# Kernel optimization log

Measured on AMD Instinct MI355X. Metric: run time of the kernel, lower is better.

Reference implementation:

```python
import jax, jax.numpy as jnp
import numpy as np
from jax import lax

B, C, H, W = 16, 256, 56, 56
MID = 16  # SE: max(C//16, 4)
EPS = 1e-5


def _bn(x, g, b, m, v):
    # inference-mode BatchNorm2d folded to per-channel scale/shift
    s = g * lax.rsqrt(v + EPS)
    return x * s[None, :, None, None] + (b - m * s)[None, :, None, None]


def _dw(x, w, ph, pw):
    # depthwise conv, NCHW, kernel w: [C,1,kh,kw]
    return lax.conv_general_dilated(
        x, w, window_strides=(1, 1), padding=[(ph, ph), (pw, pw)],
        dimension_numbers=('NCHW', 'OIHW', 'NCHW'), feature_group_count=C)


def _pw(x, w):
    # 1x1 conv, w: [O,C,1,1]
    return jnp.einsum('bchw,oc->bohw', x, w[:, :, 0, 0])


def _se(x, w1, b1, w2, b2):
    s = x.mean(axis=(2, 3))                      # [B,C] squeeze
    s = jax.nn.relu(s @ w1.T + b1)               # [B,MID]
    s = jax.nn.sigmoid(s @ w2.T + b2)            # [B,C]
    return x * s[:, :, None, None]


def setup_inputs() -> dict:
    key = jax.random.key(0)
    ks = jax.random.split(key, 32)
    rn = lambda i, shape, sc=0.05: jax.random.normal(ks[i], shape, jnp.float32) * sc
    ru = lambda i, shape: jax.random.uniform(ks[i], shape, jnp.float32)
    return {
        'x': rn(0, (B, C, H, W), 1.0),
        'pw1_w': rn(1, (C, C, 1, 1)),
        'xy3_w': rn(2, (C, 1, 3, 3)), 'xy5_w': rn(3, (C, 1, 5, 5)),
        'bnxy_g': ru(4, (C,)), 'bnxy_b': rn(5, (C,)), 'bnxy_m': rn(6, (C,)), 'bnxy_v': ru(7, (C,)),
        'xz3_w': rn(8, (C, 1, 1, 3)), 'xz5_w': rn(9, (C, 1, 1, 5)),
        'bnxz_g': ru(10, (C,)), 'bnxz_b': rn(11, (C,)), 'bnxz_m': rn(12, (C,)), 'bnxz_v': ru(13, (C,)),
        'yz3_w': rn(14, (C, 1, 3, 1)), 'yz5_w': rn(15, (C, 1, 5, 1)),
        'bnyz_g': ru(16, (C,)), 'bnyz_b': rn(17, (C,)), 'bnyz_m': rn(18, (C,)), 'bnyz_v': ru(19, (C,)),
        'alpha': jnp.full((1, C, 1, 1), 0.5, jnp.float32),
        'beta': jnp.full((1, C, 1, 1), 0.5, jnp.float32),
        'pw2_w': rn(20, (C, C, 1, 1)),
        'bn2_g': ru(21, (C,)), 'bn2_b': rn(22, (C,)), 'bn2_m': rn(23, (C,)), 'bn2_v': ru(24, (C,)),
        'fc1_w': rn(25, (MID, C)), 'fc1_b': rn(26, (MID,)),
        'fc2_w': rn(27, (C, MID)), 'fc2_b': rn(28, (C,)),
    }


def reference(x, pw1_w, xy3_w, xy5_w, bnxy_g, bnxy_b, bnxy_m, bnxy_v,
              xz3_w, xz5_w, bnxz_g, bnxz_b, bnxz_m, bnxz_v,
              yz3_w, yz5_w, bnyz_g, bnyz_b, bnyz_m, bnyz_v,
              alpha, beta, pw2_w, bn2_g, bn2_b, bn2_m, bn2_v,
              fc1_w, fc1_b, fc2_w, fc2_b):
    # Pw1: 1x1 conv, no BN / no act
    out = _pw(x, pw1_w)
    # MS_TOP (stride=1 -> pool is identity)
    # [B] xy branch: DW 3x3 + DW 5x5 -> BN -> ReLU
    f_xy = jax.nn.relu(_bn(_dw(out, xy3_w, 1, 1) + _dw(out, xy5_w, 2, 2),
                           bnxy_g, bnxy_b, bnxy_m, bnxy_v))
    # [A] xz branch: per-row depthwise Conv1d along W == depthwise (1,k) 2D conv
    f_xz = jax.nn.relu(_bn(_dw(out, xz3_w, 0, 1) + _dw(out, xz5_w, 0, 2),
                           bnxz_g, bnxz_b, bnxz_m, bnxz_v))
    # [A] yz branch: per-column depthwise Conv1d along H == depthwise (k,1) 2D conv
    f_yz = jax.nn.relu(_bn(_dw(out, yz3_w, 1, 0) + _dw(out, yz5_w, 2, 0),
                           bnyz_g, bnyz_b, bnyz_m, bnyz_v))
    # [C] learnable-gate fusion
    gate = jax.nn.sigmoid(alpha * f_xz + beta * f_yz)
    top = jax.nn.relu(f_xy * gate)
    # Pw2: 1x1 conv -> BN -> ReLU
    out2 = jax.nn.relu(_bn(_pw(top, pw2_w), bn2_g, bn2_b, bn2_m, bn2_v))
    # SE channel attention
    out2 = _se(out2, fc1_w, fc1_b, fc2_w, fc2_b)
    # DropPath is identity at inference; shortcut is identity (stride=1, in==out)
    return out2 + x
```

## Files before the change

kernel.cpp:

```cpp
#include <hip/hip_runtime.h>
#include <math.h>

typedef __bf16 bf16;
typedef __bf16 bf16x8 __attribute__((ext_vector_type(8)));
typedef __bf16 bf16x4 __attribute__((ext_vector_type(4)));
typedef float f32x4 __attribute__((ext_vector_type(4)));

#define CC 256
#define BB 16
#define HH 56
#define WW 56
#define HWSZ 3136
#define EPS 1e-5f

#define OFF_SCALE 0
#define OFF_SUMS  16384
#define OFF_WBF1  32768
#define OFF_WBF2  163840
#define OFF_WDW   294912
#define OFF_BNC   312832
#define OFF_OUT2  321024

__global__ __launch_bounds__(256) void precast(
    const float* __restrict__ w1, const float* __restrict__ w2,
    const float* __restrict__ xy3, const float* __restrict__ xy5,
    const float* __restrict__ xz3, const float* __restrict__ xz5,
    const float* __restrict__ yz3, const float* __restrict__ yz5,
    const float* __restrict__ gxy, const float* __restrict__ bxy,
    const float* __restrict__ mxy, const float* __restrict__ vxy,
    const float* __restrict__ gxz, const float* __restrict__ bxz,
    const float* __restrict__ mxz, const float* __restrict__ vxz,
    const float* __restrict__ gyz, const float* __restrict__ byz,
    const float* __restrict__ myz, const float* __restrict__ vyz,
    const float* __restrict__ alpha, const float* __restrict__ beta,
    bf16* __restrict__ wbf1, bf16* __restrict__ wbf2,
    bf16* __restrict__ wdw, float* __restrict__ bnc,
    float* __restrict__ sums)
{
    const int blk = blockIdx.x, t = threadIdx.x;
    if (blk < 128) {
        int i = blk * 512 + t * 2;
        wbf1[i] = (bf16)w1[i]; wbf1[i + 1] = (bf16)w1[i + 1];
    } else if (blk < 256) {
        int i = (blk - 128) * 512 + t * 2;
        wbf2[i] = (bf16)w2[i]; wbf2[i + 1] = (bf16)w2[i + 1];
    } else {
        const int c = t;
#pragma unroll
        for (int dh = 0; dh < 5; ++dh)
#pragma unroll
            for (int dw = 0; dw < 5; ++dw) {
                float v = xy5[c * 25 + dh * 5 + dw];
                if (dh >= 1 && dh <= 3 && dw >= 1 && dw <= 3)
                    v += xy3[c * 9 + (dh - 1) * 3 + (dw - 1)];
                wdw[(dh * 5 + dw) * CC + c] = (bf16)v;
            }
#pragma unroll
        for (int d = 0; d < 5; ++d) {
            float v = xz5[c * 5 + d];
            if (d >= 1 && d <= 3) v += xz3[c * 3 + d - 1];
            wdw[(25 + d) * CC + c] = (bf16)v;
            float u = yz5[c * 5 + d];
            if (d >= 1 && d <= 3) u += yz3[c * 3 + d - 1];
            wdw[(30 + d) * CC + c] = (bf16)u;
        }
        float s;
        s = gxy[c] * rsqrtf(vxy[c] + EPS); bnc[0*CC+c] = s; bnc[1*CC+c] = bxy[c] - mxy[c]*s;
        s = gxz[c] * rsqrtf(vxz[c] + EPS); bnc[2*CC+c] = s; bnc[3*CC+c] = bxz[c] - mxz[c]*s;
        s = gyz[c] * rsqrtf(vyz[c] + EPS); bnc[4*CC+c] = s; bnc[5*CC+c] = byz[c] - myz[c]*s;
        bnc[6*CC+c] = alpha[c]; bnc[7*CC+c] = beta[c];
        for (int i = t; i < BB * CC; i += 256) sums[i] = 0.f;
    }
}

__global__ __launch_bounds__(256, 2) void pw_gemm1(
    const float* __restrict__ in, const bf16* __restrict__ wbf,
    bf16* __restrict__ mid)
{
    __shared__ __align__(16) bf16 XT[64][264];
    const int hw0 = blockIdx.x * 64;
    const int b   = blockIdx.y;
    const int t   = threadIdx.x;
    const int lane = t & 63, wv = t >> 6;
    const int q = lane >> 4, n = lane & 15;
    const int co_w = wv * 64;

    bf16x8 aq[4][8];
#pragma unroll
    for (int cf = 0; cf < 4; ++cf) {
        const bf16* wp = wbf + (size_t)(co_w + cf * 16 + n) * CC + q * 8;
#pragma unroll
        for (int kk = 0; kk < 8; ++kk)
            aq[cf][kk] = *(const bf16x8*)(wp + kk * 32);
    }

    {
        const int hwg = (t & 15) * 4;
        const int cig = (t >> 4) * 4;
        const float* base = in + (size_t)b * CC * HWSZ + hw0 + hwg;
#pragma unroll
        for (int pass = 0; pass < 4; ++pass) {
            const int ci0 = pass * 64 + cig;
            f32x4 v[4];
#pragma unroll
            for (int i = 0; i < 4; ++i)
                v[i] = *(const f32x4*)(base + (size_t)(ci0 + i) * HWSZ);
#pragma unroll
            for (int j = 0; j < 4; ++j) {
                bf16x4 r = {(bf16)v[0][j], (bf16)v[1][j], (bf16)v[2][j], (bf16)v[3][j]};
                *(bf16x4*)(&XT[hwg + j][ci0]) = r;
            }
        }
    }
    __syncthreads();

    f32x4 acc[4][4] = {};
#pragma unroll
    for (int kk = 0; kk < 8; ++kk) {
        bf16x8 bq[4];
#pragma unroll
        for (int hf = 0; hf < 4; ++hf)
            bq[hf] = *(const bf16x8*)(&XT[hf * 16 + n][kk * 32 + q * 8]);
#pragma unroll
        for (int cf = 0; cf < 4; ++cf)
#pragma unroll
            for (int hf = 0; hf < 4; ++hf)
                acc[cf][hf] = __builtin_amdgcn_mfma_f32_16x16x32_bf16(
                    aq[cf][kk], bq[hf], acc[cf][hf], 0, 0, 0);
    }

    bf16* ob = mid + ((size_t)b * HWSZ + hw0) * CC;
#pragma unroll
    for (int cf = 0; cf < 4; ++cf) {
        const int co4 = co_w + cf * 16 + q * 4;
#pragma unroll
        for (int hf = 0; hf < 4; ++hf) {
            bf16x4 r = {(bf16)acc[cf][hf][0], (bf16)acc[cf][hf][1],
                        (bf16)acc[cf][hf][2], (bf16)acc[cf][hf][3]};
            *(bf16x4*)(ob + (size_t)(hf * 16 + n) * CC + co4) = r;
        }
    }
}

__global__ __launch_bounds__(256) void dwfuse(
    const bf16* __restrict__ mid, const bf16* __restrict__ wdw,
    const float* __restrict__ bnc, bf16* __restrict__ top)
{
    __shared__ __align__(16) bf16 lw2[35 * 512];
    const int t = threadIdx.x;
    for (int idx = t; idx < 35 * 64; idx += 256) {
        const int tap = idx >> 6, slot = idx & 63;
        *(bf16x8*)(&lw2[tap * 512 + slot * 8]) =
            *(const bf16x8*)(wdw + tap * 256 + (slot & 31) * 8);
    }
    __syncthreads();

    const int w  = blockIdx.x * 8 + (t >> 5);
    const int h0 = blockIdx.y * 2;
    const int bb = blockIdx.z;
    const int c0 = (t & 31) * 8;
    const int ls = (t & 63) * 8;
    const size_t plane = (size_t)bb * HWSZ;

    float axy[2][8] = {}, axz[2][8] = {}, ayz[2][8] = {};
#pragma unroll
    for (int dhh = 0; dhh < 6; ++dhh) {
        const int hh = h0 - 2 + dhh;
        if ((unsigned)hh >= (unsigned)HH) continue;
#pragma unroll
        for (int dw = 0; dw < 5; ++dw) {
            const int ww = w + dw - 2;
            if ((unsigned)ww >= (unsigned)WW) continue;
            bf16x8 v = *(const bf16x8*)(mid + ((plane + hh * WW + ww) * CC + c0));
            float fv[8];
#pragma unroll
            for (int j = 0; j < 8; ++j) fv[j] = (float)v[j];
#pragma unroll
            for (int p = 0; p < 2; ++p) {
                const int dh = dhh - p;
                if (dh < 0 || dh > 4) continue;
                bf16x8 wc = *(const bf16x8*)(&lw2[(dh * 5 + dw) * 512 + ls]);
#pragma unroll
                for (int j = 0; j < 8; ++j) axy[p][j] += (float)wc[j] * fv[j];
                if (dh == 2) {
                    bf16x8 wz = *(const bf16x8*)(&lw2[(25 + dw) * 512 + ls]);
#pragma unroll
                    for (int j = 0; j < 8; ++j) axz[p][j] += (float)wz[j] * fv[j];
                }
                if (dw == 2) {
                    bf16x8 wy = *(const bf16x8*)(&lw2[(30 + dh) * 512 + ls]);
#pragma unroll
                    for (int j = 0; j < 8; ++j) ayz[p][j] += (float)wy[j] * fv[j];
                }
            }
        }
    }

    float bnv[8][8];
#pragma unroll
    for (int k = 0; k < 8; ++k) {
        f32x4 a0 = *(const f32x4*)(bnc + k * CC + c0);
        f32x4 a1 = *(const f32x4*)(bnc + k * CC + c0 + 4);
#pragma unroll
        for (int j = 0; j < 4; ++j) { bnv[k][j] = a0[j]; bnv[k][4 + j] = a1[j]; }
    }

#pragma unroll
    for (int p = 0; p < 2; ++p) {
        bf16x8 r;
#pragma unroll
        for (int j = 0; j < 8; ++j) {
            const float fxy = fmaxf(axy[p][j] * bnv[0][j] + bnv[1][j], 0.f);
            const float fxz = fmaxf(axz[p][j] * bnv[2][j] + bnv[3][j], 0.f);
            const float fyz = fmaxf(ayz[p][j] * bnv[4][j] + bnv[5][j], 0.f);
            const float z   = bnv[6][j] * fxz + bnv[7][j] * fyz;
            const float g   = 1.f / (1.f + expf(-z));
            r[j] = (bf16)fmaxf(fxy * g, 0.f);
        }
        *(bf16x8*)(top + ((plane + (h0 + p) * WW + w) * CC + c0)) = r;
    }
}

__global__ __launch_bounds__(256, 2) void pw_gemm2(
    const bf16* __restrict__ top, const bf16* __restrict__ wbf,
    const float* __restrict__ g2, const float* __restrict__ b2,
    const float* __restrict__ m2, const float* __restrict__ v2,
    bf16* __restrict__ out2, float* __restrict__ sums)
{
    __shared__ __align__(16) bf16 XT[64][264];
    const int hw0 = blockIdx.x * 64;
    const int b   = blockIdx.y;
    const int t   = threadIdx.x;
    const int lane = t & 63, wv = t >> 6;
    const int q = lane >> 4, n = lane & 15;
    const int co_w = wv * 64;

    bf16x8 aq[4][8];
#pragma unroll
    for (int cf = 0; cf < 4; ++cf) {
        const bf16* wp = wbf + (size_t)(co_w + cf * 16 + n) * CC + q * 8;
#pragma unroll
        for (int kk = 0; kk < 8; ++kk)
            aq[cf][kk] = *(const bf16x8*)(wp + kk * 32);
    }

    {
        const int hw_r = t >> 2;
        const int k0   = (t & 3) * 64;
        const bf16* src = top + ((size_t)b * HWSZ + hw0 + hw_r) * CC + k0;
#pragma unroll
        for (int j = 0; j < 8; ++j)
            *(bf16x8*)(&XT[hw_r][k0 + j * 8]) = *(const bf16x8*)(src + j * 8);
    }
    __syncthreads();

    f32x4 acc[4][4] = {};
#pragma unroll
    for (int kk = 0; kk < 8; ++kk) {
        bf16x8 bq[4];
#pragma unroll
        for (int hf = 0; hf < 4; ++hf)
            bq[hf] = *(const bf16x8*)(&XT[hf * 16 + n][kk * 32 + q * 8]);
#pragma unroll
        for (int cf = 0; cf < 4; ++cf)
#pragma unroll
            for (int hf = 0; hf < 4; ++hf)
                acc[cf][hf] = __builtin_amdgcn_mfma_f32_16x16x32_bf16(
                    aq[cf][kk], bq[hf], acc[cf][hf], 0, 0, 0);
    }

    bf16* ob = out2 + ((size_t)b * HWSZ + hw0) * CC;
#pragma unroll
    for (int cf = 0; cf < 4; ++cf) {
        const int co4 = co_w + cf * 16 + q * 4;
        f32x4 g = *(const f32x4*)(g2 + co4);
        f32x4 bb = *(const f32x4*)(b2 + co4);
        f32x4 mm = *(const f32x4*)(m2 + co4);
        f32x4 vv = *(const f32x4*)(v2 + co4);
        f32x4 sc, sh;
#pragma unroll
        for (int r = 0; r < 4; ++r) {
            sc[r] = g[r] * rsqrtf(vv[r] + EPS);
            sh[r] = bb[r] - mm[r] * sc[r];
        }
        f32x4 rs = {};
#pragma unroll
        for (int hf = 0; hf < 4; ++hf) {
            bf16x4 r4;
#pragma unroll
            for (int r = 0; r < 4; ++r) {
                float v = fmaxf(acc[cf][hf][r] * sc[r] + sh[r], 0.f);
                rs[r] += v;
                r4[r] = (bf16)v;
            }
            *(bf16x4*)(ob + (size_t)(hf * 16 + n) * CC + co4) = r4;
        }
#pragma unroll
        for (int msk = 1; msk < 16; msk <<= 1)
#pragma unroll
            for (int r = 0; r < 4; ++r) rs[r] += __shfl_xor(rs[r], msk);
        if (n == 0) {
#pragma unroll
            for (int r = 0; r < 4; ++r)
                atomicAdd(&sums[b * CC + co4 + r], rs[r]);
        }
    }
}

__global__ __launch_bounds__(256) void se_fc(
    const float* __restrict__ sums,
    const float* __restrict__ w1, const float* __restrict__ b1,
    const float* __restrict__ w2, const float* __restrict__ b2,
    float* __restrict__ scale)
{
    __shared__ float mean[256];
    __shared__ float hid[16];
    const int b = blockIdx.x, tid = threadIdx.x;
    mean[tid] = sums[b * CC + tid] * (1.f / (float)HWSZ);
    __syncthreads();
    if (tid < 16) {
        float h = b1[tid];
        for (int cd = 0; cd < 256; ++cd) h += w1[tid * 256 + cd] * mean[cd];
        hid[tid] = fmaxf(h, 0.f);
    }
    __syncthreads();
    float v = b2[tid];
#pragma unroll
    for (int md = 0; md < 16; ++md) v += w2[tid * 16 + md] * hid[md];
    scale[b * CC + tid] = 1.f / (1.f + expf(-v));
}

__global__ __launch_bounds__(256) void se_apply(
    const bf16* __restrict__ out2, const float* __restrict__ x,
    const float* __restrict__ scale, float* __restrict__ out)
{
    __shared__ float TT[64 * 68];
    const int hw0 = blockIdx.x * 64;
    const int c0  = blockIdx.y * 64;
    const int b   = blockIdx.z;
    const int t   = threadIdx.x;

    {
        const int hw_r = t >> 2;
        const int coff = (t & 3) * 16;
        const bf16* p = out2 + ((size_t)b * HWSZ + hw0 + hw_r) * CC + c0 + coff;
        bf16x8 u0 = *(const bf16x8*)(p);
        bf16x8 u1 = *(const bf16x8*)(p + 8);
        const float* sp = scale + b * CC + c0 + coff;
        f32x4 s0 = *(const f32x4*)(sp), s1 = *(const f32x4*)(sp + 4);
        f32x4 s2 = *(const f32x4*)(sp + 8), s3 = *(const f32x4*)(sp + 12);
#pragma unroll
        for (int j = 0; j < 4; ++j) {
            TT[(coff + j)      * 68 + hw_r] = (float)u0[j]     * s0[j];
            TT[(coff + 4 + j)  * 68 + hw_r] = (float)u0[4 + j] * s1[j];
            TT[(coff + 8 + j)  * 68 + hw_r] = (float)u1[j]     * s2[j];
            TT[(coff + 12 + j) * 68 + hw_r] = (float)u1[4 + j] * s3[j];
        }
    }
    __syncthreads();
    {
        const int c_r   = t >> 2;
        const int hwoff = (t & 3) * 16;
        const size_t go = ((size_t)b * CC + c0 + c_r) * HWSZ + hw0 + hwoff;
#pragma unroll
        for (int v = 0; v < 4; ++v) {
            f32x4 tv = *(const f32x4*)(&TT[c_r * 68 + hwoff + v * 4]);
            f32x4 xv = *(const f32x4*)(x + go + v * 4);
#pragma unroll
            for (int j = 0; j < 4; ++j) tv[j] += xv[j];
            *(f32x4*)(out + go + v * 4) = tv;
        }
    }
}

extern "C" void kernel_launch(void* const* d_in, const int* in_sizes, int n_in,
                              void* d_out, int out_size, void* d_ws, size_t ws_size,
                              hipStream_t stream)
{
    const float* x      = (const float*)d_in[0];
    const float* pw1_w  = (const float*)d_in[1];
    const float* xy3_w  = (const float*)d_in[2];
    const float* xy5_w  = (const float*)d_in[3];
    const float* bnxy_g = (const float*)d_in[4];
    const float* bnxy_b = (const float*)d_in[5];
    const float* bnxy_m = (const float*)d_in[6];
    const float* bnxy_v = (const float*)d_in[7];
    const float* xz3_w  = (const float*)d_in[8];
    const float* xz5_w  = (const float*)d_in[9];
    const float* bnxz_g = (const float*)d_in[10];
    const float* bnxz_b = (const float*)d_in[11];
    const float* bnxz_m = (const float*)d_in[12];
    const float* bnxz_v = (const float*)d_in[13];
    const float* yz3_w  = (const float*)d_in[14];
    const float* yz5_w  = (const float*)d_in[15];
    const float* bnyz_g = (const float*)d_in[16];
    const float* bnyz_b = (const float*)d_in[17];
    const float* bnyz_m = (const float*)d_in[18];
    const float* bnyz_v = (const float*)d_in[19];
    const float* alpha  = (const float*)d_in[20];
    const float* beta   = (const float*)d_in[21];
    const float* pw2_w  = (const float*)d_in[22];
    const float* bn2_g  = (const float*)d_in[23];
    const float* bn2_b  = (const float*)d_in[24];
    const float* bn2_m  = (const float*)d_in[25];
    const float* bn2_v  = (const float*)d_in[26];
    const float* fc1_w  = (const float*)d_in[27];
    const float* fc1_b  = (const float*)d_in[28];
    const float* fc2_w  = (const float*)d_in[29];
    const float* fc2_b  = (const float*)d_in[30];

    const size_t NEL = (size_t)BB * CC * HWSZ;
    char* ws = (char*)d_ws;
    float* scale = (float*)(ws + OFF_SCALE);
    float* sums  = (float*)(ws + OFF_SUMS);
    bf16*  wbf1  = (bf16*) (ws + OFF_WBF1);
    bf16*  wbf2  = (bf16*) (ws + OFF_WBF2);
    bf16*  wdw   = (bf16*) (ws + OFF_WDW);
    float* bnc   = (float*)(ws + OFF_BNC);
    bf16*  out2  = (bf16*) (ws + OFF_OUT2);
    bf16*  mid   = (bf16*)d_out;
    bf16*  top   = (bf16*)d_out + NEL;

    precast<<<257, 256, 0, stream>>>(pw1_w, pw2_w,
        xy3_w, xy5_w, xz3_w, xz5_w, yz3_w, yz5_w,
        bnxy_g, bnxy_b, bnxy_m, bnxy_v,
        bnxz_g, bnxz_b, bnxz_m, bnxz_v,
        bnyz_g, bnyz_b, bnyz_m, bnyz_v,
        alpha, beta, wbf1, wbf2, wdw, bnc, sums);

    pw_gemm1<<<dim3(49, 16), 256, 0, stream>>>(x, wbf1, mid);
    dwfuse<<<dim3(7, 28, 16), 256, 0, stream>>>(mid, wdw, bnc, top);
    pw_gemm2<<<dim3(49, 16), 256, 0, stream>>>(top, wbf2, bn2_g, bn2_b,
                                               bn2_m, bn2_v, out2, sums);
    se_fc<<<BB, 256, 0, stream>>>(sums, fc1_w, fc1_b, fc2_w, fc2_b, scale);
    se_apply<<<dim3(49, 4, 16), 256, 0, stream>>>(out2, x, scale, (float*)d_out);
}
```

Before: 294.2 us.

## Restructure depthwise fuse kernel for 2x2 output tiles with register row reuse

Each thread now computes a 2x2 spatial tile over 4 channels instead of a 2x1 tile over 8 channels. It loads 6 neighbouring columns of a row once and reuses them across both output columns and all taps. Depthwise weights are pre-converted to fp32 in LDS so the inner loop skips per-tap bf16 conversions. The change also uses __expf and drops a redundant final ReLU. The aim is fewer global loads and less conversion work per output, at the cost of narrower 8-byte loads and more accumulator registers.

New measurement: 294.3 us. No clear change (+0.0%).

```diff
diff --git a/kernel.cpp b/kernel.cpp
--- a/kernel.cpp
+++ b/kernel.cpp
@@ -146,79 +146,94 @@
     const bf16* __restrict__ mid, const bf16* __restrict__ wdw,
     const float* __restrict__ bnc, bf16* __restrict__ top)
 {
-    __shared__ __align__(16) bf16 lw2[35 * 512];
+    __shared__ __align__(16) float lwf[35 * 256];
     const int t = threadIdx.x;
-    for (int idx = t; idx < 35 * 64; idx += 256) {
-        const int tap = idx >> 6, slot = idx & 63;
-        *(bf16x8*)(&lw2[tap * 512 + slot * 8]) =
-            *(const bf16x8*)(wdw + tap * 256 + (slot & 31) * 8);
-    }
-    __syncthreads();
-
-    const int w  = blockIdx.x * 8 + (t >> 5);
+#pragma unroll
+    for (int k = 0; k < 35; ++k)
+        lwf[k * 256 + t] = (float)wdw[k * 256 + t];
+    __syncthreads();
+
+    const int lane = t & 63;
+    const int wb = blockIdx.x * 8 + (t >> 6) * 2;
     const int h0 = blockIdx.y * 2;
-    const int bb = blockIdx.z;
-    const int c0 = (t & 31) * 8;
-    const int ls = (t & 63) * 8;
-    const size_t plane = (size_t)bb * HWSZ;
-
-    float axy[2][8] = {}, axz[2][8] = {}, ayz[2][8] = {};
+    const size_t plane = (size_t)blockIdx.z * HWSZ;
+    const int c0 = lane * 4;
+
+    f32x4 axy[2][2] = {}, axz[2][2] = {}, ayz[2][2] = {};
+
 #pragma unroll
     for (int dhh = 0; dhh < 6; ++dhh) {
         const int hh = h0 - 2 + dhh;
         if ((unsigned)hh >= (unsigned)HH) continue;
-#pragma unroll
-        for (int dw = 0; dw < 5; ++dw) {
-            const int ww = w + dw - 2;
-            if ((unsigned)ww >= (unsigned)WW) continue;
-            bf16x8 v = *(const bf16x8*)(mid + ((plane + hh * WW + ww) * CC + c0));
-            float fv[8];
-#pragma unroll
-            for (int j = 0; j < 8; ++j) fv[j] = (float)v[j];
-#pragma unroll
-            for (int p = 0; p < 2; ++p) {
-                const int dh = dhh - p;
-                if (dh < 0 || dh > 4) continue;
-                bf16x8 wc = *(const bf16x8*)(&lw2[(dh * 5 + dw) * 512 + ls]);
-#pragma unroll
-                for (int j = 0; j < 8; ++j) axy[p][j] += (float)wc[j] * fv[j];
-                if (dh == 2) {
-                    bf16x8 wz = *(const bf16x8*)(&lw2[(25 + dw) * 512 + ls]);
-#pragma unroll
-                    for (int j = 0; j < 8; ++j) axz[p][j] += (float)wz[j] * fv[j];
+        const bf16* rowp = mid + (plane + (size_t)hh * WW) * CC + c0;
+
+        f32x4 fv[6];
+#pragma unroll
+        for (int wc = 0; wc < 6; ++wc) {
+            const int ww = wb - 2 + wc;
+            f32x4 f = {0.f, 0.f, 0.f, 0.f};
+            if ((unsigned)ww < (unsigned)WW) {
+                bf16x4 v = *(const bf16x4*)(rowp + (size_t)ww * CC);
+                f[0] = (float)v[0]; f[1] = (float)v[1];
+                f[2] = (float)v[2]; f[3] = (float)v[3];
+            }
+            fv[wc] = f;
+        }
+
+#pragma unroll
+        for (int ph = 0; ph < 2; ++ph) {
+            const int dh = dhh - ph;
+            if (dh < 0 || dh > 4) continue;
+#pragma unroll
+            for (int dw = 0; dw < 5; ++dw) {
+                const f32x4 wt = *(const f32x4*)(&lwf[(dh * 5 + dw) * CC + c0]);
+                axy[ph][0] += wt * fv[dw];
+                axy[ph][1] += wt * fv[dw + 1];
+            }
+            if (dh == 2) {
+#pragma unroll
+                for (int dw = 0; dw < 5; ++dw) {
+                    const f32x4 wt = *(const f32x4*)(&lwf[(25 + dw) * CC + c0]);
+                    axz[ph][0] += wt * fv[dw];
+                    axz[ph][1] += wt * fv[dw + 1];
                 }
-                if (dw == 2) {
-                    bf16x8 wy = *(const bf16x8*)(&lw2[(30 + dh) * 512 + ls]);
-#pragma unroll
-                    for (int j = 0; j < 8; ++j) ayz[p][j] += (float)wy[j] * fv[j];
-                }
-            }
-        }
-    }
-
-    float bnv[8][8];
-#pragma unroll
-    for (int k = 0; k < 8; ++k) {
-        f32x4 a0 = *(const f32x4*)(bnc + k * CC + c0);
-        f32x4 a1 = *(const f32x4*)(bnc + k * CC + c0 + 4);
-#pragma unroll
-        for (int j = 0; j < 4; ++j) { bnv[k][j] = a0[j]; bnv[k][4 + j] = a1[j]; }
-    }
-
-#pragma unroll
-    for (int p = 0; p < 2; ++p) {
-        bf16x8 r;
-#pragma unroll
-        for (int j = 0; j < 8; ++j) {
-            const float fxy = fmaxf(axy[p][j] * bnv[0][j] + bnv[1][j], 0.f);
-            const float fxz = fmaxf(axz[p][j] * bnv[2][j] + bnv[3][j], 0.f);
-            const float fyz = fmaxf(ayz[p][j] * bnv[4][j] + bnv[5][j], 0.f);
-            const float z   = bnv[6][j] * fxz + bnv[7][j] * fyz;
-            const float g   = 1.f / (1.f + expf(-z));
-            r[j] = (bf16)fmaxf(fxy * g, 0.f);
-        }
-        *(bf16x8*)(top + ((plane + (h0 + p) * WW + w) * CC + c0)) = r;
-    }
+            }
+            {
+                const f32x4 wt = *(const f32x4*)(&lwf[(30 + dh) * CC + c0]);
+                ayz[ph][0] += wt * fv[2];
+                ayz[ph][1] += wt * fv[3];
+            }
+        }
+    }
+
+    const f32x4 sxy = *(const f32x4*)(bnc + 0 * CC + c0);
+    const f32x4 hxy = *(const f32x4*)(bnc + 1 * CC + c0);
+    const f32x4 sxz = *(const f32x4*)(bnc + 2 * CC + c0);
+    const f32x4 hxz = *(const f32x4*)(bnc + 3 * CC + c0);
+    const f32x4 syz = *(const f32x4*)(bnc + 4 * CC + c0);
+    const f32x4 hyz = *(const f32x4*)(bnc + 5 * CC + c0);
+    const f32x4 al  = *(const f32x4*)(bnc + 6 * CC + c0);
+    const f32x4 be  = *(const f32x4*)(bnc + 7 * CC + c0);
+
+#pragma unroll
+    for (int ph = 0; ph < 2; ++ph)
+#pragma unroll
+        for (int pw = 0; pw < 2; ++pw) {
+            const f32x4 txy = axy[ph][pw] * sxy + hxy;
+            const f32x4 txz = axz[ph][pw] * sxz + hxz;
+            const f32x4 tyz = ayz[ph][pw] * syz + hyz;
+            bf16x4 r;
+#pragma unroll
+            for (int j = 0; j < 4; ++j) {
+                const float fxy = fmaxf(txy[j], 0.f);
+                const float fxz = fmaxf(txz[j], 0.f);
+                const float fyz = fmaxf(tyz[j], 0.f);
+                const float z   = al[j] * fxz + be[j] * fyz;
+                const float g   = 1.f / (1.f + __expf(-z));
+                r[j] = (bf16)(fxy * g);
+            }
+            *(bf16x4*)(top + (plane + (size_t)(h0 + ph) * WW + (wb + pw)) * CC + c0) = r;
+        }
 }
 
 __global__ __launch_bounds__(256, 2) void pw_gemm2(
```
